# Performance work log

Hardware: AMD Instinct MI355X
Metric: run time of the kernel (lower is better)

Reference implementation:

```python
import jax, jax.numpy as jnp
import numpy as np

B, T, H, I, O, L = 8, 8192, 256, 256, 256, 2


def setup_inputs() -> dict:
    key = jax.random.key(0)
    ks = jax.random.split(key, 12)
    s = 1.0 / np.sqrt(H)
    inp = {
        "emb": jax.random.normal(ks[0], (B, T, I), jnp.float32),
        "start": jax.random.randint(ks[1], (B, T), 0, 2) > 0,  # bool reset flags
        "h0": jnp.zeros((L, B, H), jnp.float32),               # per-layer initial carry
        "min_w": jax.random.normal(ks[2], (H, I), jnp.float32) * s,
        "min_b": jnp.zeros((H,), jnp.float32),
        "mout_w": jax.random.normal(ks[3], (O, H), jnp.float32) * s,
        "mout_b": jnp.zeros((O,), jnp.float32),
        "Wf_w": jax.random.normal(ks[4], (L, H, H), jnp.float32) * s,
        "Wf_b": jnp.zeros((L, H), jnp.float32),
        "Wh_w": jax.random.normal(ks[5], (L, H, H), jnp.float32) * s,
        "Wh_b": jnp.zeros((L, H), jnp.float32),
        "Uf_w": jax.random.normal(ks[6], (L, H, H), jnp.float32) * s,
        "Uh_w": jax.random.normal(ks[7], (L, H, H), jnp.float32) * s,
        "ff_w": jax.random.normal(ks[8], (L, H, H), jnp.float32) * s,
        "ff_b": jnp.zeros((L, H), jnp.float32),
    }
    return inp


def reference(emb, start, h0, min_w, min_b, mout_w, mout_b,
              Wf_w, Wf_b, Wh_w, Wh_b, Uf_w, Uh_w, ff_w, ff_b):
    # map_in: [B,T,I] -> [B,T,H]
    x = jnp.einsum('bti,hi->bth', emb, min_w) + min_b
    start_t = start.T  # [T,B]
    h_final = []
    for l in range(L):
        # Precompute input-side projections outside the scan (time-parallel).
        xf = jnp.einsum('bth,oh->bto', x, Wf_w[l]) + Wf_b[l]  # [B,T,H]
        xh = jnp.einsum('bth,oh->bto', x, Wh_w[l]) + Wh_b[l]  # [B,T,H]
        Uf = Uf_w[l]
        Uh = Uh_w[l]

        def step(h, inp):
            xft, xht, st = inp  # [B,H], [B,H], [B]
            # Resettable: zero the carry where a new episode starts.
            h = jnp.where(st[:, None], jnp.zeros_like(h), h)
            f = jax.nn.sigmoid(xft + h @ Uf.T)
            h_hat = jnp.tanh(xht + (f * h) @ Uh.T)
            h_new = (1.0 - f) * h + f * h_hat
            return h_new, h_new

        hT, z = jax.lax.scan(step, h0[l],
                             (xf.transpose(1, 0, 2), xh.transpose(1, 0, 2), start_t))
        h_final.append(hT)
        z = z.transpose(1, 0, 2)  # [B,T,H]
        # per-layer feedforward + leaky_relu (slope 0.01)
        x = jax.nn.leaky_relu(jnp.einsum('bth,oh->bto', z, ff_w[l]) + ff_b[l])
    out = jnp.einsum('bth,oh->bto', x, mout_w) + mout_b  # [B,T,O]
    return out, jnp.stack(h_final)  # ([B,T,O], [L,B,H])
```

## Files before the change

kernel.cpp:

```cpp
#include <hip/hip_runtime.h>
#include <hip/hip_fp16.h>
#include <cstdint>
#include <cstddef>

#define BATCH 8
#define TT 8192
#define HD 256
#define RTOT (BATCH * TT)
#define HC 16
#define NPAIR (TT / (2 * HC))

typedef __attribute__((ext_vector_type(4))) float    f32x4;
typedef __attribute__((ext_vector_type(8))) _Float16 f16x8;
typedef __attribute__((ext_vector_type(4))) _Float16 f16x4;

typedef __attribute__((address_space(1))) const void gvoid_t;
typedef __attribute__((address_space(3))) void lvoid_t;

__device__ __forceinline__ void gl_lds16(const void* g, void* l) {
  __builtin_amdgcn_global_load_lds((gvoid_t*)g, (lvoid_t*)l, 16, 0, 0);
}

__device__ __forceinline__ void ldsbar() {
  asm volatile("s_waitcnt lgkmcnt(0)" ::: "memory");
  __builtin_amdgcn_s_barrier();
}

__global__ void detect_start_par(const unsigned int* __restrict__ s,
                                 int* __restrict__ bad) {
  const unsigned int w = s[blockIdx.x * blockDim.x + threadIdx.x];
  const unsigned int b0 = w & 255u, b1 = (w >> 8) & 255u,
                     b2 = (w >> 16) & 255u, b3 = (w >> 24) & 255u;
  const int bi = (b1 | b2 | b3) != 0;
  const int bf = (b0 != 0) || (b1 != 0) ||
                 (b2 != 0 && b2 != 0x80u) || (b3 != 0 && b3 != 0x3fu);
  if (__any(bi) && (threadIdx.x & 63) == 0) atomicOr(&bad[0], 1);
  if (__any(bf) && (threadIdx.x & 63) == 0) atomicOr(&bad[1], 1);
}

__global__ void conv_f16(const float* __restrict__ in, _Float16* __restrict__ out,
                         const int n) {
  const int i = (blockIdx.x * blockDim.x + threadIdx.x) * 8;
  if (i + 7 >= n) return;
  const float4 a = *(const float4*)&in[i];
  const float4 b = *(const float4*)&in[i + 4];
  f16x8 v;
  v[0] = (_Float16)a.x; v[1] = (_Float16)a.y; v[2] = (_Float16)a.z; v[3] = (_Float16)a.w;
  v[4] = (_Float16)b.x; v[5] = (_Float16)b.y; v[6] = (_Float16)b.z; v[7] = (_Float16)b.w;
  *(f16x8*)&out[i] = v;
}

__global__ void conv_w8(const float* p0, const float* p1, const float* p2,
                        const float* p3, const float* p4, const float* p5,
                        const float* p6, const float* p7,
                        _Float16* __restrict__ out) {
  const int seg = blockIdx.y;
  const float* p;
  switch (seg) {
    case 0: p = p0; break; case 1: p = p1; break;
    case 2: p = p2; break; case 3: p = p3; break;
    case 4: p = p4; break; case 5: p = p5; break;
    case 6: p = p6; break; default: p = p7; break;
  }
  const int i = (blockIdx.x * blockDim.x + threadIdx.x) * 8;
  const float4 a = *(const float4*)&p[i];
  const float4 b = *(const float4*)&p[i + 4];
  f16x8 v;
  v[0] = (_Float16)a.x; v[1] = (_Float16)a.y; v[2] = (_Float16)a.z; v[3] = (_Float16)a.w;
  v[4] = (_Float16)b.x; v[5] = (_Float16)b.y; v[6] = (_Float16)b.z; v[7] = (_Float16)b.w;
  *(f16x8*)&out[(size_t)seg * 65536 + i] = v;
}

__global__ void swz_w(const float* __restrict__ Uf, const float* __restrict__ Uh,
                      _Float16* __restrict__ outp) {
  const int gid  = blockIdx.x * 256 + threadIdx.x;
  const int lane = gid & 63;
  const int w    = (gid >> 6) & 7;
  const int f    = (gid >> 9) & 15;
  const int mat  = (gid >> 13) & 1;
  const int l    = gid >> 14;
  const int fr = lane & 15, fq = lane >> 4;
  const int tile = f >> 3, kc = f & 7;
  const int nrow = (w * 2 + tile) * 16 + fr;
  const int kb   = kc * 32 + fq * 8;
  const float* src = (mat ? Uh : Uf) + (size_t)l * 65536 + nrow * 256 + kb;
  const float4 a = *(const float4*)src;
  const float4 b = *(const float4*)(src + 4);
  f16x8 v;
  v[0] = (_Float16)a.x; v[1] = (_Float16)a.y; v[2] = (_Float16)a.z; v[3] = (_Float16)a.w;
  v[4] = (_Float16)b.x; v[5] = (_Float16)b.y; v[6] = (_Float16)b.z; v[7] = (_Float16)b.w;
  *(f16x8*)&outp[(size_t)gid * 8] = v;
}

__global__ __launch_bounds__(256, 4) void gemm_h(
    const _Float16* __restrict__ A, const _Float16* __restrict__ W,
    const float* __restrict__ bias, _Float16* __restrict__ C16,
    float* __restrict__ C32, const int act) {
  __shared__ __align__(16) char smem[34816];
  _Float16* As = (_Float16*)smem;
  _Float16* Ws = (_Float16*)(smem + 8192);
  _Float16* EP = (_Float16*)smem;

  const int tid  = threadIdx.x;
  const int wave = tid >> 6, lane = tid & 63;
  const int wm = wave >> 1, wn = wave & 1;
  const int bm = blockIdx.x * 128, bn = blockIdx.y * 128;
  const int lrow  = tid >> 2;
  const int lcol8 = (tid & 3) * 8;
  const int fr = lane & 15;
  const int fq = lane >> 4;

  f32x4 acc[4][4];
#pragma unroll
  for (int i = 0; i < 4; i++)
#pragma unroll
    for (int j = 0; j < 4; j++) acc[i][j] = (f32x4){0.f, 0.f, 0.f, 0.f};

  float bv[4];
#pragma unroll
  for (int ni = 0; ni < 4; ni++) bv[ni] = bias[bn + wn * 64 + ni * 16 + fr];

  for (int k0 = 0; k0 < HD; k0 += 32) {
    __syncthreads();
#pragma unroll
    for (int is = 0; is < 2; is++) {
      gl_lds16(&A[(size_t)(bm + is * 64 + lrow) * HD + k0 + lcol8],
               smem + wave * 1024 + is * 4096);
      gl_lds16(&W[(size_t)(bn + is * 64 + lrow) * HD + k0 + lcol8],
               smem + 8192 + wave * 1024 + is * 4096);
    }
    asm volatile("s_waitcnt vmcnt(0)" ::: "memory");
    __syncthreads();
    f16x8 af[4], bf[4];
#pragma unroll
    for (int mi = 0; mi < 4; mi++)
      af[mi] = *(const f16x8*)(As + (wm * 64 + mi * 16 + fr) * 32 + fq * 8);
#pragma unroll
    for (int ni = 0; ni < 4; ni++)
      bf[ni] = *(const f16x8*)(Ws + (wn * 64 + ni * 16 + fr) * 32 + fq * 8);
#pragma unroll
    for (int mi = 0; mi < 4; mi++)
#pragma unroll
      for (int ni = 0; ni < 4; ni++)
        acc[mi][ni] = __builtin_amdgcn_mfma_f32_16x16x32_f16(af[mi], bf[ni],
                                                             acc[mi][ni], 0, 0, 0);
  }
  __syncthreads();

  if (C32) {
#pragma unroll
    for (int mi = 0; mi < 4; mi++)
#pragma unroll
      for (int ni = 0; ni < 4; ni++)
#pragma unroll
        for (int j = 0; j < 4; j++) {
          float v = acc[mi][ni][j] + bv[ni];
          if (act == 1) v = (v > 0.f) ? v : 0.01f * v;
          C32[(size_t)(bm + wm * 64 + mi * 16 + fq * 4 + j) * HD +
              bn + wn * 64 + ni * 16 + fr] = v;
        }
  } else {
#pragma unroll
    for (int mi = 0; mi < 4; mi++)
#pragma unroll
      for (int ni = 0; ni < 4; ni++)
#pragma unroll
        for (int j = 0; j < 4; j++) {
          float v = acc[mi][ni][j] + bv[ni];
          if (act == 1) v = (v > 0.f) ? v : 0.01f * v;
          EP[(wm * 64 + mi * 16 + fq * 4 + j) * 136 + wn * 64 + ni * 16 + fr] =
              (_Float16)v;
        }
    __syncthreads();
#pragma unroll
    for (int ps = 0; ps < 8; ps++) {
      const int row = ps * 16 + (tid >> 4);
      const f16x8 v = *(const f16x8*)(EP + row * 136 + (tid & 15) * 8);
      *(f16x8*)&C16[(size_t)(bm + row) * HD + bn + (tid & 15) * 8] = v;
    }
  }
}

__global__ __launch_bounds__(256, 2) void gemm_dual(
    const _Float16* __restrict__ A,
    const _Float16* __restrict__ W1, const _Float16* __restrict__ W2,
    const float* __restrict__ b1, const float* __restrict__ b2,
    _Float16* __restrict__ C1, _Float16* __restrict__ C2) {
  __shared__ __align__(16) char smem[34816];
  _Float16* As  = (_Float16*)smem;
  _Float16* Ws1 = (_Float16*)(smem + 8192);
  _Float16* Ws2 = (_Float16*)(smem + 16384);
  _Float16* EP  = (_Float16*)smem;

  const int tid  = threadIdx.x;
  const int wave = tid >> 6, lane = tid & 63;
  const int wm = wave >> 1, wn = wave & 1;
  const int bm = blockIdx.x * 128, bn = blockIdx.y * 128;
  const int lrow  = tid >> 2;
  const int lcol8 = (tid & 3) * 8;
  const int fr = lane & 15;
  const int fq = lane >> 4;

  f32x4 acc1[4][4], acc2[4][4];
#pragma unroll
  for (int i = 0; i < 4; i++)
#pragma unroll
    for (int j = 0; j < 4; j++) {
      acc1[i][j] = (f32x4){0.f, 0.f, 0.f, 0.f};
      acc2[i][j] = (f32x4){0.f, 0.f, 0.f, 0.f};
    }

  float bv1[4], bv2[4];
#pragma unroll
  for (int ni = 0; ni < 4; ni++) {
    bv1[ni] = b1[bn + wn * 64 + ni * 16 + fr];
    bv2[ni] = b2[bn + wn * 64 + ni * 16 + fr];
  }

  for (int k0 = 0; k0 < HD; k0 += 32) {
    __syncthreads();
#pragma unroll
    for (int is = 0; is < 2; is++) {
      gl_lds16(&A[(size_t)(bm + is * 64 + lrow) * HD + k0 + lcol8],
               smem + wave * 1024 + is * 4096);
      gl_lds16(&W1[(size_t)(bn + is * 64 + lrow) * HD + k0 + lcol8],
               smem + 8192 + wave * 1024 + is * 4096);
      gl_lds16(&W2[(size_t)(bn + is * 64 + lrow) * HD + k0 + lcol8],
               smem + 16384 + wave * 1024 + is * 4096);
    }
    asm volatile("s_waitcnt vmcnt(0)" ::: "memory");
    __syncthreads();
    f16x8 af[4], bf1[4], bf2[4];
#pragma unroll
    for (int mi = 0; mi < 4; mi++)
      af[mi] = *(const f16x8*)(As + (wm * 64 + mi * 16 + fr) * 32 + fq * 8);
#pragma unroll
    for (int ni = 0; ni < 4; ni++) {
      bf1[ni] = *(const f16x8*)(Ws1 + (wn * 64 + ni * 16 + fr) * 32 + fq * 8);
      bf2[ni] = *(const f16x8*)(Ws2 + (wn * 64 + ni * 16 + fr) * 32 + fq * 8);
    }
#pragma unroll
    for (int mi = 0; mi < 4; mi++)
#pragma unroll
      for (int ni = 0; ni < 4; ni++) {
        acc1[mi][ni] = __builtin_amdgcn_mfma_f32_16x16x32_f16(af[mi], bf1[ni],
                                                              acc1[mi][ni], 0, 0, 0);
        acc2[mi][ni] = __builtin_amdgcn_mfma_f32_16x16x32_f16(af[mi], bf2[ni],
                                                              acc2[mi][ni], 0, 0, 0);
      }
  }

#pragma unroll
  for (int which = 0; which < 2; which++) {
    __syncthreads();
#pragma unroll
    for (int mi = 0; mi < 4; mi++)
#pragma unroll
      for (int ni = 0; ni < 4; ni++)
#pragma unroll
        for (int j = 0; j < 4; j++) {
          const float v = (which == 0 ? acc1[mi][ni][j] + bv1[ni]
                                      : acc2[mi][ni][j] + bv2[ni]);
          EP[(wm * 64 + mi * 16 + fq * 4 + j) * 136 + wn * 64 + ni * 16 + fr] =
              (_Float16)v;
        }
    __syncthreads();
    _Float16* Cd = (which == 0) ? C1 : C2;
#pragma unroll
    for (int ps = 0; ps < 8; ps++) {
      const int row = ps * 16 + (tid >> 4);
      const f16x8 v = *(const f16x8*)(EP + row * 136 + (tid & 15) * 8);
      *(f16x8*)&Cd[(size_t)(bm + row) * HD + bn + (tid & 15) * 8] = v;
    }
  }
}

__global__ __launch_bounds__(512) void scan_mgu(
    const _Float16* __restrict__ xf, const _Float16* __restrict__ xh,
    const void* __restrict__ startp, const int* __restrict__ badf,
    const float* __restrict__ h0l,
    const _Float16* __restrict__ wfrag,
    _Float16* __restrict__ z, float* __restrict__ hfin) {
  const int tid  = threadIdx.x;
  const int wave = tid >> 6;
  const int lane = tid & 63;
  const int fr   = lane & 15;
  const int fq   = lane >> 4;
  const int col  = fr;
  const int b    = col & 7;
  const int grp  = col >> 3;
  const int base = blockIdx.x * (2 * HC);
  const int t0c  = base + grp * HC;
  const int mode = (!badf[0]) ? 1 : (!badf[1] ? 2 : 0);

  __shared__ __align__(16) char hbuf[8192];
  __shared__ __align__(16) char gbuf[8192];
  __shared__ int rb[16];

  auto flag = [&](int bb, int t) -> int {
    const int idx = bb * TT + t;
    if (mode == 1) return ((const int*)startp)[idx] != 0;
    if (mode == 2) return ((const float*)startp)[idx] != 0.0f;
    return ((const uint8_t*)startp)[idx] != 0;
  };
  auto ldfrag = [&](const char* buf, int kc) -> f16x8 {
    int off = kc * 1024 + fq * 256 + fr * 16;
    off ^= ((off >> 8) & 1) << 4;
    return *(const f16x8*)(buf + off);
  };
  auto stfrag = [&](char* buf, int nb, const float4 v) {
    int off = ((nb >> 5) * 1024) + (((nb >> 3) & 3) * 256) + col * 16 + (nb & 7) * 2;
    off ^= ((off >> 8) & 1) << 4;
    f16x4 p;
    p[0] = (_Float16)v.x; p[1] = (_Float16)v.y;
    p[2] = (_Float16)v.z; p[3] = (_Float16)v.w;
    *(f16x4*)(buf + off) = p;
  };

  f16x8 auf[2][8], auh[2][8];
#pragma unroll
  for (int f = 0; f < 16; f++)
    auf[f >> 3][f & 7] =
        *(const f16x8*)&wfrag[((size_t)(f * 512) + wave * 64 + lane) * 8];
#pragma unroll
  for (int f = 0; f < 16; f++)
    auh[f >> 3][f & 7] =
        *(const f16x8*)&wfrag[((size_t)(8192 + f * 512) + wave * 64 + lane) * 8];

  if (tid < 16) rb[tid] = -1;
  __syncthreads();
  {
    const int cg  = tid >> 5;
    const int l32 = tid & 31;
    const int t0g = base + (cg >> 3) * HC;
    const int bg  = cg & 7;
    for (int off = 0;; off += 32) {
      const int st = t0g - off - l32;
      if (st >= 0 && rb[cg] < 0 && flag(bg, st)) atomicMax(&rb[cg], st);
      __syncthreads();
      bool done = true;
#pragma unroll
      for (int c = 0; c < 16; c++) {
        const int tc = base + (c >> 3) * HC;
        if (rb[c] < 0 && tc - off >= 0) done = false;
      }
      if (done) break;
      __syncthreads();
    }
  }
  __syncthreads();

  const int rbc    = rb[col];
  const int startc = max(rbc, 0);
  int Lmax = 0;
#pragma unroll
  for (int c = 0; c < 16; c++) {
    const int tc = base + (c >> 3) * HC;
    const int s  = max(rb[c], 0);
    Lmax = max(Lmax, tc - s);
  }

  const int nb0 = (wave * 2 + 0) * 16 + fq * 4;
  const int nb1 = (wave * 2 + 1) * 16 + fq * 4;

  float4 hinit0 = make_float4(0.f, 0.f, 0.f, 0.f), hinit1 = hinit0;
  if (rbc < 0) {
    hinit0 = *(const float4*)&h0l[b * HD + nb0];
    hinit1 = *(const float4*)&h0l[b * HD + nb1];
  }
  float4 hr0 = hinit0, hr1 = hinit1;
  stfrag(hbuf, nb0, hr0);
  stfrag(hbuf, nb1, hr1);
  __syncthreads();

  int t = t0c - Lmax;
  int tcl = min(max(t, 0), TT - 1);
  f16x4 pxf0 = *(const f16x4*)&xf[((size_t)b * TT + tcl) * HD + nb0];
  f16x4 pxf1 = *(const f16x4*)&xf[((size_t)b * TT + tcl) * HD + nb1];
  f16x4 pxh0 = *(const f16x4*)&xh[((size_t)b * TT + tcl) * HD + nb0];
  f16x4 pxh1 = *(const f16x4*)&xh[((size_t)b * TT + tcl) * HD + nb1];
  int fnext = (t + 1 < TT) ? flag(b, max(t + 1, 0)) : 0;

  for (int i = -Lmax; i < HC; i++) {
    t = t0c + i;
    f32x4 cf0 = {(float)pxf0[0], (float)pxf0[1], (float)pxf0[2], (float)pxf0[3]};
    f32x4 cf1 = {(float)pxf1[0], (float)pxf1[1], (float)pxf1[2], (float)pxf1[3]};
    f32x4 ch0 = {(float)pxh0[0], (float)pxh0[1], (float)pxh0[2], (float)pxh0[3]};
    f32x4 ch1 = {(float)pxh1[0], (float)pxh1[1], (float)pxh1[2], (float)pxh1[3]};

    const int fcur = fnext;
    const int tn = min(max(t + 1, 0), TT - 1);
    pxf0 = *(const f16x4*)&xf[((size_t)b * TT + tn) * HD + nb0];
    pxf1 = *(const f16x4*)&xf[((size_t)b * TT + tn) * HD + nb1];
    pxh0 = *(const f16x4*)&xh[((size_t)b * TT + tn) * HD + nb0];
    pxh1 = *(const f16x4*)&xh[((size_t)b * TT + tn) * HD + nb1];
    fnext = (t + 2 < TT) ? flag(b, max(t + 2, 0)) : 0;

    int stn = 0;
    if (t + 1 <= startc) stn = 2;
    else if (fcur) stn = 1;

#pragma unroll
    for (int kc = 0; kc < 8; kc++) {
      const f16x8 bv = ldfrag(hbuf, kc);
      cf0 = __builtin_amdgcn_mfma_f32_16x16x32_f16(auf[0][kc], bv, cf0, 0, 0, 0);
      cf1 = __builtin_amdgcn_mfma_f32_16x16x32_f16(auf[1][kc], bv, cf1, 0, 0, 0);
    }
    f32x4 fv0, fv1;
    float4 g0, g1;
#pragma unroll
    for (int r = 0; r < 4; r++) {
      const float f0 = 1.f / (1.f + __expf(-cf0[r]));
      const float f1 = 1.f / (1.f + __expf(-cf1[r]));
      fv0[r] = f0; fv1[r] = f1;
      (&g0.x)[r] = f0 * (&hr0.x)[r];
      (&g1.x)[r] = f1 * (&hr1.x)[r];
    }
    stfrag(gbuf, nb0, g0);
    stfrag(gbuf, nb1, g1);
    ldsbar();

#pragma unroll
    for (int kc = 0; kc < 8; kc++) {
      const f16x8 bv = ldfrag(gbuf, kc);
      ch0 = __builtin_amdgcn_mfma_f32_16x16x32_f16(auh[0][kc], bv, ch0, 0, 0, 0);
      ch1 = __builtin_amdgcn_mfma_f32_16x16x32_f16(auh[1][kc], bv, ch1, 0, 0, 0);
    }
    float4 hn0, hn1;
    f16x4 zn0, zn1;
#pragma unroll
    for (int r = 0; r < 4; r++) {
      const float e0 = __expf(2.f * ch0[r]);
      const float e1 = __expf(2.f * ch1[r]);
      const float hh0 = 1.f - 2.f / (e0 + 1.f);
      const float hh1 = 1.f - 2.f / (e1 + 1.f);
      (&hn0.x)[r] = (1.f - fv0[r]) * (&hr0.x)[r] + fv0[r] * hh0;
      (&hn1.x)[r] = (1.f - fv1[r]) * (&hr1.x)[r] + fv1[r] * hh1;
      zn0[r] = (_Float16)(&hn0.x)[r];
      zn1[r] = (_Float16)(&hn1.x)[r];
    }
    if (i >= 0) {
      *(f16x4*)&z[((size_t)b * TT + t) * HD + nb0] = zn0;
      *(f16x4*)&z[((size_t)b * TT + t) * HD + nb1] = zn1;
    }
    if (t == TT - 1) {
      *(float4*)&hfin[b * HD + nb0] = hn0;
      *(float4*)&hfin[b * HD + nb1] = hn1;
    }
    hr0 = (stn == 2) ? hinit0 : (stn == 1 ? make_float4(0.f, 0.f, 0.f, 0.f) : hn0);
    hr1 = (stn == 2) ? hinit1 : (stn == 1 ? make_float4(0.f, 0.f, 0.f, 0.f) : hn1);
    stfrag(hbuf, nb0, hr0);
    stfrag(hbuf, nb1, hr1);
    ldsbar();
  }
}

extern "C" void kernel_launch(void* const* d_in, const int* in_sizes, int n_in,
                              void* d_out, int out_size, void* d_ws, size_t ws_size,
                              hipStream_t stream) {
  const float* emb    = (const float*)d_in[0];
  const void*  startp = d_in[1];
  const float* h0     = (const float*)d_in[2];
  const float* min_w  = (const float*)d_in[3];
  const float* min_b  = (const float*)d_in[4];
  const float* mout_w = (const float*)d_in[5];
  const float* mout_b = (const float*)d_in[6];
  const float* Wf_w   = (const float*)d_in[7];
  const float* Wf_b   = (const float*)d_in[8];
  const float* Wh_w   = (const float*)d_in[9];
  const float* Wh_b   = (const float*)d_in[10];
  const float* Uf_w   = (const float*)d_in[11];
  const float* Uh_w   = (const float*)d_in[12];
  const float* ff_w   = (const float*)d_in[13];
  const float* ff_b   = (const float*)d_in[14];

  float* out = (float*)d_out;
  char*  ws  = (char*)d_ws;
  int*   bad = (int*)ws;
  _Float16* w16  = (_Float16*)(ws + 1024);
  _Float16* uswz = (_Float16*)(ws + 1024 + 8 * 65536 * 2);
  _Float16* bufE = (_Float16*)(ws + 1024 + 8 * 65536 * 2 + 524288);
  _Float16* bufA = bufE + (size_t)RTOT * HD;
  _Float16* bufB = bufA + (size_t)RTOT * HD;
  _Float16* bufC = bufB + (size_t)RTOT * HD;
  float* hfin = out + (size_t)RTOT * HD;
  const size_t WO = (size_t)HD * HD;

  _Float16* w_min = w16;
  _Float16* w_out = w16 + 1 * WO;
  _Float16* w_f0  = w16 + 2 * WO;
  _Float16* w_f1  = w16 + 3 * WO;
  _Float16* w_h0  = w16 + 4 * WO;
  _Float16* w_h1  = w16 + 5 * WO;
  _Float16* w_ff0 = w16 + 6 * WO;
  _Float16* w_ff1 = w16 + 7 * WO;

  hipMemsetAsync(bad, 0, 16, stream);
  detect_start_par<<<64, 256, 0, stream>>>((const unsigned int*)startp, bad);
  conv_f16<<<RTOT * HD / 2048, 256, 0, stream>>>(emb, bufE, RTOT * HD);
  conv_w8<<<dim3(32, 8), 256, 0, stream>>>(min_w, mout_w, Wf_w, Wf_w + WO,
                                           Wh_w, Wh_w + WO, ff_w, ff_w + WO, w16);
  swz_w<<<128, 256, 0, stream>>>(Uf_w, Uh_w, uswz);

  const dim3 gg(RTOT / 128, HD / 128);
  gemm_h<<<gg, 256, 0, stream>>>(bufE, w_min, min_b, bufA, nullptr, 0);
  gemm_dual<<<gg, 256, 0, stream>>>(bufA, w_f0, w_h0, Wf_b, Wh_b, bufB, bufC);
  scan_mgu<<<NPAIR, 512, 0, stream>>>(bufB, bufC, startp, bad, h0,
                                      uswz, bufA, hfin);
  gemm_h<<<gg, 256, 0, stream>>>(bufA, w_ff0, ff_b, bufB, nullptr, 1);
  gemm_dual<<<gg, 256, 0, stream>>>(bufB, w_f1, w_h1, Wf_b + HD, Wh_b + HD, bufC, bufA);
  scan_mgu<<<NPAIR, 512, 0, stream>>>(bufC, bufA, startp, bad, h0 + BATCH * HD,
                                      uswz + (size_t)16384 * 8, bufB, hfin + BATCH * HD);
  gemm_h<<<gg, 256, 0, stream>>>(bufB, w_ff1, ff_b + HD, bufA, nullptr, 1);
  gemm_h<<<gg, 256, 0, stream>>>(bufA, w_out, mout_b, nullptr, out, 0);
}
```

Before: 367.7 us.

## Split scan into two 512-thread teams per block with halved time chunks

```diff
diff --git a/kernel.cpp b/kernel.cpp
--- a/kernel.cpp
+++ b/kernel.cpp
@@ -7,8 +7,8 @@
 #define TT 8192
 #define HD 256
 #define RTOT (BATCH * TT)
-#define HC 16
-#define NPAIR (TT / (2 * HC))
+#define HC 8
+#define SCAN_WG (TT / (4 * HC))
 
 typedef __attribute__((ext_vector_type(4))) float    f32x4;
 typedef __attribute__((ext_vector_type(8))) _Float16 f16x8;
@@ -275,27 +275,28 @@
   }
 }
 
-__global__ __launch_bounds__(512) void scan_mgu(
+__global__ __launch_bounds__(1024, 4) void scan_mgu(
     const _Float16* __restrict__ xf, const _Float16* __restrict__ xh,
     const void* __restrict__ startp, const int* __restrict__ badf,
     const float* __restrict__ h0l,
     const _Float16* __restrict__ wfrag,
     _Float16* __restrict__ z, float* __restrict__ hfin) {
   const int tid  = threadIdx.x;
-  const int wave = tid >> 6;
+  const int team = tid >> 9;
+  const int twv  = (tid >> 6) & 7;
   const int lane = tid & 63;
   const int fr   = lane & 15;
   const int fq   = lane >> 4;
-  const int col  = fr;
-  const int b    = col & 7;
-  const int grp  = col >> 3;
-  const int base = blockIdx.x * (2 * HC);
-  const int t0c  = base + grp * HC;
+  const int b    = fr & 7;
+  const int grp  = fr >> 3;
+  const int base = blockIdx.x * (4 * HC);
+  const int t0c  = base + (team * 2 + grp) * HC;
   const int mode = (!badf[0]) ? 1 : (!badf[1] ? 2 : 0);
 
-  __shared__ __align__(16) char hbuf[8192];
-  __shared__ __align__(16) char gbuf[8192];
-  __shared__ int rb[16];
+  __shared__ __align__(16) char lds[32768];
+  __shared__ int rb[32];
+  char* hbuf = lds + team * 16384;
+  char* gbuf = hbuf + 8192;
 
   auto flag = [&](int bb, int t) -> int {
     const int idx = bb * TT + t;
@@ -309,7 +310,7 @@
     return *(const f16x8*)(buf + off);
   };
   auto stfrag = [&](char* buf, int nb, const float4 v) {
-    int off = ((nb >> 5) * 1024) + (((nb >> 3) & 3) * 256) + col * 16 + (nb & 7) * 2;
+    int off = ((nb >> 5) * 1024) + (((nb >> 3) & 3) * 256) + fr * 16 + (nb & 7) * 2;
     off ^= ((off >> 8) & 1) << 4;
     f16x4 p;
     p[0] = (_Float16)v.x; p[1] = (_Float16)v.y;
@@ -321,13 +322,13 @@
 #pragma unroll
   for (int f = 0; f < 16; f++)
     auf[f >> 3][f & 7] =
-        *(const f16x8*)&wfrag[((size_t)(f * 512) + wave * 64 + lane) * 8];
+        *(const f16x8*)&wfrag[((size_t)(f * 512) + twv * 64 + lane) * 8];
 #pragma unroll
   for (int f = 0; f < 16; f++)
     auh[f >> 3][f & 7] =
-        *(const f16x8*)&wfrag[((size_t)(8192 + f * 512) + wave * 64 + lane) * 8];
-
-  if (tid < 16) rb[tid] = -1;
+        *(const f16x8*)&wfrag[((size_t)(8192 + f * 512) + twv * 64 + lane) * 8];
+
+  if (tid < 32) rb[tid] = -1;
   __syncthreads();
   {
     const int cg  = tid >> 5;
@@ -340,7 +341,7 @@
       __syncthreads();
       bool done = true;
 #pragma unroll
-      for (int c = 0; c < 16; c++) {
+      for (int c = 0; c < 32; c++) {
         const int tc = base + (c >> 3) * HC;
         if (rb[c] < 0 && tc - off >= 0) done = false;
       }
@@ -350,18 +351,18 @@
   }
   __syncthreads();
 
-  const int rbc    = rb[col];
+  const int rbc    = rb[(team * 2 + grp) * 8 + b];
   const int startc = max(rbc, 0);
   int Lmax = 0;
 #pragma unroll
-  for (int c = 0; c < 16; c++) {
+  for (int c = 0; c < 32; c++) {
     const int tc = base + (c >> 3) * HC;
     const int s  = max(rb[c], 0);
     Lmax = max(Lmax, tc - s);
   }
 
-  const int nb0 = (wave * 2 + 0) * 16 + fq * 4;
-  const int nb1 = (wave * 2 + 1) * 16 + fq * 4;
+  const int nb0 = (twv * 2 + 0) * 16 + fq * 4;
+  const int nb1 = (twv * 2 + 1) * 16 + fq * 4;
 
   float4 hinit0 = make_float4(0.f, 0.f, 0.f, 0.f), hinit1 = hinit0;
   if (rbc < 0) {
@@ -505,12 +506,12 @@
   const dim3 gg(RTOT / 128, HD / 128);
   gemm_h<<<gg, 256, 0, stream>>>(bufE, w_min, min_b, bufA, nullptr, 0);
   gemm_dual<<<gg, 256, 0, stream>>>(bufA, w_f0, w_h0, Wf_b, Wh_b, bufB, bufC);
-  scan_mgu<<<NPAIR, 512, 0, stream>>>(bufB, bufC, startp, bad, h0,
-                                      uswz, bufA, hfin);
+  scan_mgu<<<SCAN_WG, 1024, 0, stream>>>(bufB, bufC, startp, bad, h0,
+                                         uswz, bufA, hfin);
   gemm_h<<<gg, 256, 0, stream>>>(bufA, w_ff0, ff_b, bufB, nullptr, 1);
   gemm_dual<<<gg, 256, 0, stream>>>(bufB, w_f1, w_h1, Wf_b + HD, Wh_b + HD, bufC, bufA);
-  scan_mgu<<<NPAIR, 512, 0, stream>>>(bufC, bufA, startp, bad, h0 + BATCH * HD,
-                                      uswz + (size_t)16384 * 8, bufB, hfin + BATCH * HD);
+  scan_mgu<<<SCAN_WG, 1024, 0, stream>>>(bufC, bufA, startp, bad, h0 + BATCH * HD,
+                                         uswz + (size_t)16384 * 8, bufB, hfin + BATCH * HD);
   gemm_h<<<gg, 256, 0, stream>>>(bufB, w_ff1, ff_b + HD, bufA, nullptr, 1);
   gemm_h<<<gg, 256, 0, stream>>>(bufA, w_out, mout_b, nullptr, out, 0);
 }
```

Result: slower. 834.9 us (+127.1%).

## Double-buffer LDS staging in GEMMs and swizzle block order across 1D grid

Applied to the files above, without the earlier changes.

```diff
diff --git a/kernel.cpp b/kernel.cpp
--- a/kernel.cpp
+++ b/kernel.cpp
@@ -97,14 +97,13 @@
     const float* __restrict__ bias, _Float16* __restrict__ C16,
     float* __restrict__ C32, const int act) {
   __shared__ __align__(16) char smem[34816];
-  _Float16* As = (_Float16*)smem;
-  _Float16* Ws = (_Float16*)(smem + 8192);
   _Float16* EP = (_Float16*)smem;
 
   const int tid  = threadIdx.x;
   const int wave = tid >> 6, lane = tid & 63;
   const int wm = wave >> 1, wn = wave & 1;
-  const int bm = blockIdx.x * 128, bn = blockIdx.y * 128;
+  const int swz  = (blockIdx.x & 7) * 128 + (blockIdx.x >> 3);
+  const int bm = (swz >> 1) * 128, bn = (swz & 1) * 128;
   const int lrow  = tid >> 2;
   const int lcol8 = (tid & 3) * 8;
   const int fr = lane & 15;
@@ -120,17 +119,28 @@
 #pragma unroll
   for (int ni = 0; ni < 4; ni++) bv[ni] = bias[bn + wn * 64 + ni * 16 + fr];
 
-  for (int k0 = 0; k0 < HD; k0 += 32) {
-    __syncthreads();
+  auto STAGE = [&](int kk, int bb) {
+    const int k0 = kk * 32;
 #pragma unroll
     for (int is = 0; is < 2; is++) {
       gl_lds16(&A[(size_t)(bm + is * 64 + lrow) * HD + k0 + lcol8],
-               smem + wave * 1024 + is * 4096);
+               smem + bb * 16384 + wave * 1024 + is * 4096);
       gl_lds16(&W[(size_t)(bn + is * 64 + lrow) * HD + k0 + lcol8],
-               smem + 8192 + wave * 1024 + is * 4096);
-    }
-    asm volatile("s_waitcnt vmcnt(0)" ::: "memory");
-    __syncthreads();
+               smem + bb * 16384 + 8192 + wave * 1024 + is * 4096);
+    }
+  };
+
+  STAGE(0, 0);
+#pragma unroll
+  for (int k = 0; k < 8; k++) {
+    const int cur = k & 1;
+    STAGE(k < 7 ? k + 1 : 7, cur ^ 1);
+    asm volatile("s_waitcnt vmcnt(4)" ::: "memory");
+    __builtin_amdgcn_s_barrier();
+    __builtin_amdgcn_sched_barrier(0);
+    asm volatile("" ::: "memory");
+    const _Float16* As = (const _Float16*)(smem + cur * 16384);
+    const _Float16* Ws = (const _Float16*)(smem + cur * 16384 + 8192);
     f16x8 af[4], bf[4];
 #pragma unroll
     for (int mi = 0; mi < 4; mi++)
@@ -144,6 +154,10 @@
       for (int ni = 0; ni < 4; ni++)
         acc[mi][ni] = __builtin_amdgcn_mfma_f32_16x16x32_f16(af[mi], bf[ni],
                                                              acc[mi][ni], 0, 0, 0);
+    asm volatile("s_waitcnt lgkmcnt(0)" ::: "memory");
+    __builtin_amdgcn_s_barrier();
+    __builtin_amdgcn_sched_barrier(0);
+    asm volatile("" ::: "memory");
   }
   __syncthreads();
 
@@ -186,16 +200,14 @@
     const _Float16* __restrict__ W1, const _Float16* __restrict__ W2,
     const float* __restrict__ b1, const float* __restrict__ b2,
     _Float16* __restrict__ C1, _Float16* __restrict__ C2) {
-  __shared__ __align__(16) char smem[34816];
-  _Float16* As  = (_Float16*)smem;
-  _Float16* Ws1 = (_Float16*)(smem + 8192);
-  _Float16* Ws2 = (_Float16*)(smem + 16384);
-  _Float16* EP  = (_Float16*)smem;
+  __shared__ __align__(16) char smem[49152];
+  _Float16* EP = (_Float16*)smem;
 
   const int tid  = threadIdx.x;
   const int wave = tid >> 6, lane = tid & 63;
   const int wm = wave >> 1, wn = wave & 1;
-  const int bm = blockIdx.x * 128, bn = blockIdx.y * 128;
+  const int swz  = (blockIdx.x & 7) * 128 + (blockIdx.x >> 3);
+  const int bm = (swz >> 1) * 128, bn = (swz & 1) * 128;
   const int lrow  = tid >> 2;
   const int lcol8 = (tid & 3) * 8;
   const int fr = lane & 15;
@@ -217,19 +229,31 @@
     bv2[ni] = b2[bn + wn * 64 + ni * 16 + fr];
   }
 
-  for (int k0 = 0; k0 < HD; k0 += 32) {
-    __syncthreads();
+  auto STAGE = [&](int kk, int bb) {
+    const int k0 = kk * 32;
 #pragma unroll
     for (int is = 0; is < 2; is++) {
       gl_lds16(&A[(size_t)(bm + is * 64 + lrow) * HD + k0 + lcol8],
-               smem + wave * 1024 + is * 4096);
+               smem + bb * 24576 + wave * 1024 + is * 4096);
       gl_lds16(&W1[(size_t)(bn + is * 64 + lrow) * HD + k0 + lcol8],
-               smem + 8192 + wave * 1024 + is * 4096);
+               smem + bb * 24576 + 8192 + wave * 1024 + is * 4096);
       gl_lds16(&W2[(size_t)(bn + is * 64 + lrow) * HD + k0 + lcol8],
-               smem + 16384 + wave * 1024 + is * 4096);
-    }
-    asm volatile("s_waitcnt vmcnt(0)" ::: "memory");
-    __syncthreads();
+               smem + bb * 24576 + 16384 + wave * 1024 + is * 4096);
+    }
+  };
+
+  STAGE(0, 0);
+#pragma unroll
+  for (int k = 0; k < 8; k++) {
+    const int cur = k & 1;
+    STAGE(k < 7 ? k + 1 : 7, cur ^ 1);
+    asm volatile("s_waitcnt vmcnt(6)" ::: "memory");
+    __builtin_amdgcn_s_barrier();
+    __builtin_amdgcn_sched_barrier(0);
+    asm volatile("" ::: "memory");
+    const _Float16* As  = (const _Float16*)(smem + cur * 24576);
+    const _Float16* Ws1 = (const _Float16*)(smem + cur * 24576 + 8192);
+    const _Float16* Ws2 = (const _Float16*)(smem + cur * 24576 + 16384);
     f16x8 af[4], bf1[4], bf2[4];
 #pragma unroll
     for (int mi = 0; mi < 4; mi++)
@@ -248,6 +272,10 @@
         acc2[mi][ni] = __builtin_amdgcn_mfma_f32_16x16x32_f16(af[mi], bf2[ni],
                                                               acc2[mi][ni], 0, 0, 0);
       }
+    asm volatile("s_waitcnt lgkmcnt(0)" ::: "memory");
+    __builtin_amdgcn_s_barrier();
+    __builtin_amdgcn_sched_barrier(0);
+    asm volatile("" ::: "memory");
   }
 
 #pragma unroll
@@ -502,15 +530,14 @@
                                            Wh_w, Wh_w + WO, ff_w, ff_w + WO, w16);
   swz_w<<<128, 256, 0, stream>>>(Uf_w, Uh_w, uswz);
 
-  const dim3 gg(RTOT / 128, HD / 128);
-  gemm_h<<<gg, 256, 0, stream>>>(bufE, w_min, min_b, bufA, nullptr, 0);
-  gemm_dual<<<gg, 256, 0, stream>>>(bufA, w_f0, w_h0, Wf_b, Wh_b, bufB, bufC);
+  gemm_h<<<1024, 256, 0, stream>>>(bufE, w_min, min_b, bufA, nullptr, 0);
+  gemm_dual<<<1024, 256, 0, stream>>>(bufA, w_f0, w_h0, Wf_b, Wh_b, bufB, bufC);
   scan_mgu<<<NPAIR, 512, 0, stream>>>(bufB, bufC, startp, bad, h0,
                                       uswz, bufA, hfin);
-  gemm_h<<<gg, 256, 0, stream>>>(bufA, w_ff0, ff_b, bufB, nullptr, 1);
-  gemm_dual<<<gg, 256, 0, stream>>>(bufB, w_f1, w_h1, Wf_b + HD, Wh_b + HD, bufC, bufA);
+  gemm_h<<<1024, 256, 0, stream>>>(bufA, w_ff0, ff_b, bufB, nullptr, 1);
+  gemm_dual<<<1024, 256, 0, stream>>>(bufB, w_f1, w_h1, Wf_b + HD, Wh_b + HD, bufC, bufA);
   scan_mgu<<<NPAIR, 512, 0, stream>>>(bufC, bufA, startp, bad, h0 + BATCH * HD,
                                       uswz + (size_t)16384 * 8, bufB, hfin + BATCH * HD);
-  gemm_h<<<gg, 256, 0, stream>>>(bufB, w_ff1, ff_b + HD, bufA, nullptr, 1);
-  gemm_h<<<gg, 256, 0, stream>>>(bufA, w_out, mout_b, nullptr, out, 0);
-}
+  gemm_h<<<1024, 256, 0, stream>>>(bufB, w_ff1, ff_b + HD, bufA, nullptr, 1);
+  gemm_h<<<1024, 256, 0, stream>>>(bufA, w_out, mout_b, nullptr, out, 0);
+}
```

Result: no change. 363.7 us (-1.1%).
